# Kernel tuning notes

Measured on AMD Instinct MI355X. Metric: run time of the kernel, lower is better.

Reference implementation:

```python
import jax, jax.numpy as jnp
import numpy as np

M, K, N = 8192, 4096, 4096

def setup_inputs() -> dict:
    key = jax.random.key(0)
    k0, k1, k2, k3, k4 = jax.random.split(key, 5)
    x = jax.random.normal(k0, (M, K), dtype=jnp.float32)
    # int8 weight stored as int32 spec dtype; values in [-127, 127]
    weight = jax.random.randint(k1, (N, K), -127, 128, dtype=jnp.int32)
    input_scale = jnp.array([0.02], dtype=jnp.float32)
    input_offset = jnp.zeros((1,), dtype=jnp.int32)
    # per-output-channel dequant scale (small positive)
    deq_scale = jax.random.uniform(k2, (N,), dtype=jnp.float32, minval=1e-4, maxval=2e-4)
    quant_bias = jax.random.randint(k3, (N,), -100, 101, dtype=jnp.int32)
    # sparse-compression output-channel reorder index (a permutation)
    index = jax.random.permutation(k4, N).astype(jnp.int32)
    return {"x": x, "weight": weight, "input_scale": input_scale,
            "input_offset": input_offset, "deq_scale": deq_scale,
            "quant_bias": quant_bias, "index": index}

def reference(x, weight, input_scale, input_offset, deq_scale, quant_bias, index):
    # 1) per-tensor activation quantization to int8
    x_q = jnp.clip(jnp.round(x / input_scale) + input_offset.astype(jnp.float32),
                   -128.0, 127.0).astype(jnp.int8)
    acc = jnp.matmul(x_q.astype(jnp.int32), weight.astype(jnp.int8).astype(jnp.int32).T)
    acc = acc + quant_bias  # [M, N] int32
    # 3) per-channel dequantization
    y = acc.astype(jnp.float32) * deq_scale  # [M, N]
    # 4) restore output-channel order from compressed layout
    return jnp.take(y, index, axis=-1)
```

## Files before the change

kernel.cpp:

```cpp
#include <hip/hip_runtime.h>
#include <hip/hip_bf16.h>
#include <stdint.h>

#define M_DIM 8192
#define K_DIM 4096
#define N_DIM 4096

#define BM 256
#define BN 256
#define BKB 64
#define NT (K_DIM / BKB)
#define ATILE (BM * BKB)
#define BTILE (BN * BKB)

typedef int i32x4 __attribute__((ext_vector_type(4)));

__global__ __launch_bounds__(256) void quant_x_kernel(
    const float* __restrict__ x, const float* __restrict__ scale_p,
    const int* __restrict__ off_p, int8_t* __restrict__ xq)
{
    const float s = scale_p[0];
    const float off = (float)off_p[0];
    long base = ((long)blockIdx.x * 256 + threadIdx.x) * 16;
    const float4* xin = (const float4*)(x + base);
    float v[16];
    *(float4*)(v + 0)  = xin[0];
    *(float4*)(v + 4)  = xin[1];
    *(float4*)(v + 8)  = xin[2];
    *(float4*)(v + 12) = xin[3];
    uint32_t pk[4];
#pragma unroll
    for (int g = 0; g < 4; ++g) {
        uint32_t p = 0;
#pragma unroll
        for (int j = 0; j < 4; ++j) {
            float q = rintf(v[g * 4 + j] / s) + off;
            q = fminf(fmaxf(q, -128.0f), 127.0f);
            int qi = (int)q;
            p |= ((uint32_t)(qi & 0xff)) << (8 * j);
        }
        pk[g] = p;
    }
    uint4 o; o.x = pk[0]; o.y = pk[1]; o.z = pk[2]; o.w = pk[3];
    *(uint4*)(xq + base) = o;
}

__global__ __launch_bounds__(256) void pack_w_kernel(
    const int* __restrict__ w, const int* __restrict__ index,
    const float* __restrict__ deq, const int* __restrict__ qb,
    int8_t* __restrict__ bp, float* __restrict__ dsp, int* __restrict__ qbp)
{
    int j = blockIdx.x;
    int t = threadIdx.x;
    int src = index[j];
    const int4* wrow = (const int4*)(w + (long)src * K_DIM);
    uint32_t pk[4];
#pragma unroll
    for (int g = 0; g < 4; ++g) {
        int4 c = wrow[t * 4 + g];
        pk[g] = ((uint32_t)(c.x & 0xff)) | (((uint32_t)(c.y & 0xff)) << 8) |
                (((uint32_t)(c.z & 0xff)) << 16) | (((uint32_t)(c.w & 0xff)) << 24);
    }
    uint4 o; o.x = pk[0]; o.y = pk[1]; o.z = pk[2]; o.w = pk[3];
    *(uint4*)(bp + (long)j * K_DIM + t * 16) = o;
    if (t == 0) { dsp[j] = deq[src]; qbp[j] = qb[src]; }
}

__device__ __forceinline__ void gload_lds16(const int8_t* g, int8_t* l)
{
    __builtin_amdgcn_global_load_lds(
        (const __attribute__((address_space(1))) uint32_t*)g,
        (__attribute__((address_space(3))) uint32_t*)l, 16, 0, 0);
}

__global__ __launch_bounds__(512, 2) void gemm_i8_kernel(
    const int8_t* __restrict__ A, const int8_t* __restrict__ B,
    const float* __restrict__ dsp, const int* __restrict__ qbp,
    float* __restrict__ C)
{
    __shared__ int8_t lds[3][ATILE + BTILE];

    int bid = blockIdx.x;
    int swz = (bid & 7) * (gridDim.x >> 3) + (bid >> 3);
    int bm = swz & 31;
    int bn = swz >> 5;
    int brow = bm * BM, bcol = bn * BN;

    int t = threadIdx.x;
    int wv = t >> 6;
    int l  = t & 63;
    int lr = l & 15;
    int ls = l >> 4;
    int wrM = (wv >> 2) * 128;
    int wcN = (wv & 3) * 64;
    int pslot = ls ^ ((lr >> 1) & 3);

    int aoff[8], boff[4];
#pragma unroll
    for (int m = 0; m < 8; ++m)
        aoff[m] = (wrM + m * 16 + lr) * BKB + pslot * 16;
#pragma unroll
    for (int n = 0; n < 4; ++n)
        boff[n] = ATILE + (wcN + n * 16 + lr) * BKB + pslot * 16;

    const int8_t* sa[2]; int da[2];
    const int8_t* sb[2]; int db[2];
#pragma unroll
    for (int i = 0; i < 2; ++i) {
        int ca = i * 512 + t;
        int row = ca >> 2;
        int lg = (ca & 3) ^ ((row >> 1) & 3);
        sa[i] = A + (long)(brow + row) * K_DIM + lg * 16;
        da[i] = ca * 16;
        sb[i] = B + (long)(bcol + row) * K_DIM + lg * 16;
        db[i] = ATILE + ca * 16;
    }

#pragma unroll
    for (int p = 0; p < 2; ++p) {
        gload_lds16(sa[0], &lds[p][da[0]]);
        gload_lds16(sa[1], &lds[p][da[1]]);
        gload_lds16(sb[0], &lds[p][db[0]]);
        gload_lds16(sb[1], &lds[p][db[1]]);
        sa[0] += BKB; sa[1] += BKB; sb[0] += BKB; sb[1] += BKB;
    }
    asm volatile("s_waitcnt vmcnt(4)" ::: "memory");
    __builtin_amdgcn_s_barrier();

    i32x4 acc[8][4] = {};

    for (int kt = 0; kt < NT; ++kt) {
        const int cur = kt % 3;
        const int stg = (kt + 2) % 3;
        const bool do_stage = (kt + 2) < NT;
        const int8_t* base = lds[cur];

        i32x4 af[4], bf[4];

#pragma unroll
        for (int n = 0; n < 4; ++n) bf[n] = *(const i32x4*)(base + boff[n]);
#pragma unroll
        for (int m = 0; m < 4; ++m) af[m] = *(const i32x4*)(base + aoff[m]);
        if (do_stage) {
            gload_lds16(sa[0], &lds[stg][da[0]]);
            gload_lds16(sa[1], &lds[stg][da[1]]);
            sa[0] += BKB; sa[1] += BKB;
        }
        __builtin_amdgcn_s_barrier();
        asm volatile("s_waitcnt lgkmcnt(0)" ::: "memory");
        __builtin_amdgcn_sched_barrier(0);
        __builtin_amdgcn_s_setprio(1);
#pragma unroll
        for (int m = 0; m < 4; ++m)
#pragma unroll
            for (int n = 0; n < 4; ++n)
                acc[m][n] = __builtin_amdgcn_mfma_i32_16x16x64_i8(
                    af[m], bf[n], acc[m][n], 0, 0, 0);
        __builtin_amdgcn_s_setprio(0);
        __builtin_amdgcn_s_barrier();

#pragma unroll
        for (int m = 0; m < 4; ++m) af[m] = *(const i32x4*)(base + aoff[m + 4]);
        if (do_stage) {
            gload_lds16(sb[0], &lds[stg][db[0]]);
            gload_lds16(sb[1], &lds[stg][db[1]]);
            sb[0] += BKB; sb[1] += BKB;
        }
        __builtin_amdgcn_s_barrier();
        asm volatile("s_waitcnt lgkmcnt(0)" ::: "memory");
        __builtin_amdgcn_sched_barrier(0);
        __builtin_amdgcn_s_setprio(1);
#pragma unroll
        for (int m = 0; m < 4; ++m)
#pragma unroll
            for (int n = 0; n < 4; ++n)
                acc[m + 4][n] = __builtin_amdgcn_mfma_i32_16x16x64_i8(
                    af[m], bf[n], acc[m + 4][n], 0, 0, 0);
        __builtin_amdgcn_s_setprio(0);
        if (do_stage) asm volatile("s_waitcnt vmcnt(4)" ::: "memory");
        else          asm volatile("s_waitcnt vmcnt(0)" ::: "memory");
        __builtin_amdgcn_s_barrier();
    }

#pragma unroll
    for (int n = 0; n < 4; ++n) {
        int gc = bcol + wcN + n * 16 + lr;
        float ds = dsp[gc];
        int qb = qbp[gc];
#pragma unroll
        for (int m = 0; m < 8; ++m) {
            int gr0 = brow + wrM + m * 16 + ls * 4;
#pragma unroll
            for (int r = 0; r < 4; ++r) {
                C[(long)(gr0 + r) * N_DIM + gc] = (float)(acc[m][n][r] + qb) * ds;
            }
        }
    }
}

extern "C" void kernel_launch(void* const* d_in, const int* in_sizes, int n_in,
                              void* d_out, int out_size, void* d_ws, size_t ws_size,
                              hipStream_t stream)
{
    (void)in_sizes; (void)n_in; (void)out_size; (void)ws_size;
    const float* x   = (const float*)d_in[0];
    const int*   w   = (const int*)d_in[1];
    const float* is  = (const float*)d_in[2];
    const int*   io  = (const int*)d_in[3];
    const float* dq  = (const float*)d_in[4];
    const int*   qb  = (const int*)d_in[5];
    const int*   idx = (const int*)d_in[6];
    float* out = (float*)d_out;

    int8_t* xq  = (int8_t*)d_ws;
    int8_t* bp  = xq + (size_t)M_DIM * K_DIM;
    float*  dsp = (float*)(bp + (size_t)N_DIM * K_DIM);
    int*    qbp = (int*)(dsp + N_DIM);

    long quant_blocks = ((long)M_DIM * K_DIM) / 16 / 256;
    quant_x_kernel<<<(int)quant_blocks, 256, 0, stream>>>(x, is, io, xq);
    pack_w_kernel<<<N_DIM, 256, 0, stream>>>(w, idx, dq, qb, bp, dsp, qbp);
    gemm_i8_kernel<<<(M_DIM / BM) * (N_DIM / BN), 512, 0, stream>>>(xq, bp, dsp, qbp, out);
}
```

Measured before the change: 201.6 us.

## Merge two half-iterations of GEMM main loop into one with single barrier

Collapses the two-phase k-iteration (two A-halves each with its own barriers) into a single phase that loads all 8 A fragments and issues all four staged global-to-LDS loads at once, removing three of four workgroup barriers per k-step. It also replaces the modulo-3 buffer indexing with incrementing counters. The intent is less barrier and synchronisation overhead per iteration, at the cost of more live VGPRs for fragments and losing the interleaving of LDS reads with MFMA across halves. The vmcnt(4) wait is now counted against a single group of four loads per stage.

```diff
diff --git a/kernel.cpp b/kernel.cpp
--- a/kernel.cpp
+++ b/kernel.cpp
@@ -128,58 +128,41 @@
     __builtin_amdgcn_s_barrier();
 
     i32x4 acc[8][4] = {};
+    int cur = 0, stg = 2;
 
     for (int kt = 0; kt < NT; ++kt) {
-        const int cur = kt % 3;
-        const int stg = (kt + 2) % 3;
         const bool do_stage = (kt + 2) < NT;
         const int8_t* base = lds[cur];
 
-        i32x4 af[4], bf[4];
-
+        i32x4 af[8], bf[4];
 #pragma unroll
         for (int n = 0; n < 4; ++n) bf[n] = *(const i32x4*)(base + boff[n]);
 #pragma unroll
-        for (int m = 0; m < 4; ++m) af[m] = *(const i32x4*)(base + aoff[m]);
+        for (int m = 0; m < 8; ++m) af[m] = *(const i32x4*)(base + aoff[m]);
         if (do_stage) {
-            gload_lds16(sa[0], &lds[stg][da[0]]);
-            gload_lds16(sa[1], &lds[stg][da[1]]);
-            sa[0] += BKB; sa[1] += BKB;
+            int8_t* sdst = lds[stg];
+            gload_lds16(sa[0], sdst + da[0]);
+            gload_lds16(sa[1], sdst + da[1]);
+            gload_lds16(sb[0], sdst + db[0]);
+            gload_lds16(sb[1], sdst + db[1]);
+            sa[0] += BKB; sa[1] += BKB; sb[0] += BKB; sb[1] += BKB;
         }
-        __builtin_amdgcn_s_barrier();
         asm volatile("s_waitcnt lgkmcnt(0)" ::: "memory");
         __builtin_amdgcn_sched_barrier(0);
         __builtin_amdgcn_s_setprio(1);
 #pragma unroll
-        for (int m = 0; m < 4; ++m)
+        for (int m = 0; m < 8; ++m)
 #pragma unroll
             for (int n = 0; n < 4; ++n)
                 acc[m][n] = __builtin_amdgcn_mfma_i32_16x16x64_i8(
                     af[m], bf[n], acc[m][n], 0, 0, 0);
         __builtin_amdgcn_s_setprio(0);
-        __builtin_amdgcn_s_barrier();
-
-#pragma unroll
-        for (int m = 0; m < 4; ++m) af[m] = *(const i32x4*)(base + aoff[m + 4]);
-        if (do_stage) {
-            gload_lds16(sb[0], &lds[stg][db[0]]);
-            gload_lds16(sb[1], &lds[stg][db[1]]);
-            sb[0] += BKB; sb[1] += BKB;
-        }
-        __builtin_amdgcn_s_barrier();
-        asm volatile("s_waitcnt lgkmcnt(0)" ::: "memory");
         __builtin_amdgcn_sched_barrier(0);
-        __builtin_amdgcn_s_setprio(1);
-#pragma unroll
-        for (int m = 0; m < 4; ++m)
-#pragma unroll
-            for (int n = 0; n < 4; ++n)
-                acc[m + 4][n] = __builtin_amdgcn_mfma_i32_16x16x64_i8(
-                    af[m], bf[n], acc[m + 4][n], 0, 0, 0);
-        __builtin_amdgcn_s_setprio(0);
         if (do_stage) asm volatile("s_waitcnt vmcnt(4)" ::: "memory");
         else          asm volatile("s_waitcnt vmcnt(0)" ::: "memory");
         __builtin_amdgcn_s_barrier();
+        cur = (cur == 2) ? 0 : cur + 1;
+        stg = (stg == 2) ? 0 : stg + 1;
     }
 
 #pragma unroll
```

New measurement: 197.2 us. 2.2% less time.
